# Optimization experiments

Hardware: AMD Instinct MI355X
Metric: run time of the kernel (lower is better)

Reference implementation:

```python
import jax, jax.numpy as jnp
import numpy as np

B, C, H, W = 4, 64, 64, 64
CI = C // 2  # inter_channels


def setup_inputs() -> dict:
    key = jax.random.key(0)
    k1, k2, k3, k4, k5 = jax.random.split(key, 5)
    x = jax.random.normal(k1, (B, C, H, W), dtype=jnp.float32)
    # 1x1 conv g: in C -> CI (weight [CI, C], bias [CI])
    Wg = jax.random.normal(k2, (CI, C), dtype=jnp.float32) * (1.0 / np.sqrt(C))
    bg = jax.random.normal(k3, (CI,), dtype=jnp.float32) * 0.01
    # 1x1 conv W_z: CI -> C
    Wz = jax.random.normal(k4, (C, CI), dtype=jnp.float32) * (1.0 / np.sqrt(CI))
    bz = jax.random.normal(k5, (C,), dtype=jnp.float32) * 0.01
    return {"x": x, "Wg": Wg, "bg": bg, "Wz": Wz, "bz": bz}


def reference(x, Wg, bg, Wz, bz):
    b, c, h, w = x.shape
    n = h * w
    xf = x.reshape(b, c, n)                       # [B,C,N]
    # g projection (1x1 conv) then flatten: [B,N,CI]
    g_x = jnp.einsum('bcn,oc->bno', xf, Wg) + bg  # [B,N,CI]
    # theta = phi = raw x flattened
    theta = xf.transpose(0, 2, 1)                 # [B,N,C]
    f = jnp.einsum('bnc,bcm->bnm', theta, xf)     # [B,N,N]
    f_div_C = jax.nn.softmax(f, axis=-1)
    y = jnp.einsum('bnm,bmo->bno', f_div_C, g_x)  # [B,N,CI]
    y = y.transpose(0, 2, 1).reshape(b, CI, h, w)  # [B,CI,H,W]
    # W_z projection (1x1 conv) + residual
    W_y = jnp.einsum('oi,bihw->bohw', Wz, y) + bz[None, :, None, None]
    return W_y + x
```

## Files before the change

kernel.cpp:

```cpp
#include <hip/hip_runtime.h>
#include <hip/hip_bf16.h>
#include <math.h>

#define B_  4
#define C_  64
#define N_  4096
#define CI_ 32

typedef __attribute__((ext_vector_type(8))) unsigned short u16x8;
typedef __attribute__((ext_vector_type(8))) __bf16        bf16x8;
typedef __attribute__((ext_vector_type(4))) __bf16        bf16x4;
typedef __attribute__((ext_vector_type(4))) float         f32x4;

__device__ __forceinline__ unsigned short f2bf(float f) {
    union { float f; unsigned int i; } v; v.f = f;
    unsigned int r = v.i + 0x7FFFu + ((v.i >> 16) & 1u);
    return (unsigned short)(r >> 16);
}

__global__ __launch_bounds__(256) void k_prep(
    const float* __restrict__ x, const float* __restrict__ Wg,
    const float* __restrict__ bg, unsigned short* __restrict__ xT,
    unsigned short* __restrict__ gx, float* __restrict__ diag)
{
    __shared__ __align__(16) float tile[64][68];
    __shared__ float part[4][64][33];
    const int t  = threadIdx.x;
    const int b  = blockIdx.x >> 6;
    const int n0 = (blockIdx.x & 63) * 64;

    #pragma unroll
    for (int pass = 0; pass < 4; ++pass) {
        int c   = (t >> 4) + pass * 16;
        int nl4 = (t & 15) * 4;
        float4 v = *(const float4*)(x + (size_t)(b * C_ + c) * N_ + n0 + nl4);
        *(float4*)&tile[c][nl4] = v;
    }
    __syncthreads();

    {
        const int n  = t >> 2;
        const int cc = (t & 3) * 16;
        u16x8 a, b2;
        #pragma unroll
        for (int j = 0; j < 8; ++j) a[j]  = f2bf(tile[cc + j][n]);
        #pragma unroll
        for (int j = 0; j < 8; ++j) b2[j] = f2bf(tile[cc + 8 + j][n]);
        unsigned short* dst = xT + (size_t)(b * N_ + n0 + n) * C_ + cc;
        *(u16x8*)dst       = a;
        *(u16x8*)(dst + 8) = b2;
    }
    {
        const int nl = t & 63, cq = t >> 6;
        float acc[CI_];
        #pragma unroll
        for (int o = 0; o < CI_; ++o) acc[o] = 0.f;
        float dd = 0.f;
        #pragma unroll 4
        for (int cl = 0; cl < 16; ++cl) {
            int c = cq * 16 + cl;
            float xv = tile[c][nl];
            dd += xv * xv;
            #pragma unroll
            for (int o = 0; o < CI_; ++o) acc[o] += Wg[o * C_ + c] * xv;
        }
        #pragma unroll
        for (int o = 0; o < CI_; ++o) part[cq][nl][o] = acc[o];
        part[cq][nl][32] = dd;
    }
    __syncthreads();
    {
        const int o = t >> 3, nr = (t & 7) * 8;
        u16x8 w;
        #pragma unroll
        for (int j = 0; j < 8; ++j) {
            int n = nr + j;
            float s = part[0][n][o] + part[1][n][o] + part[2][n][o] + part[3][n][o]
                    + bg[o];
            w[j] = f2bf(s);
        }
        *(u16x8*)(gx + (size_t)(b * CI_ + o) * N_ + n0 + nr) = w;
    }
    if (t < 64)
        diag[(size_t)b * N_ + n0 + t] =
            part[0][t][32] + part[1][t][32] + part[2][t][32] + part[3][t][32];
}

__device__ __forceinline__ f32x4 mfma16(bf16x8 a, bf16x8 b, f32x4 c) {
    return __builtin_amdgcn_mfma_f32_16x16x32_bf16(a, b, c, 0, 0, 0);
}

#define LOADA(Adst, koff)                                                      \
    _Pragma("unroll")                                                          \
    for (int kt = 0; kt < 2; ++kt) {                                           \
        _Pragma("unroll")                                                      \
        for (int kc = 0; kc < 2; ++kc)                                         \
            Adst[kt][kc] = *(const bf16x8*)(aBase                              \
                + (size_t)((koff) + kt * 16) * C_ + kc * 32);                  \
    }

#define LOADB(Bdst, koff)                                                      \
    Bdst[0] = *(const bf16x8*)(bBase0 + (koff));                               \
    Bdst[1] = *(const bf16x8*)(bBase1 + (koff));

#define TILE(Ar, Br, POFF)                                                     \
    {                                                                          \
        f32x4 S[2][2];                                                         \
        _Pragma("unroll")                                                      \
        for (int kt = 0; kt < 2; ++kt) {                                       \
            _Pragma("unroll")                                                  \
            for (int qt = 0; qt < 2; ++qt) {                                   \
                f32x4 z = (f32x4){nKq[qt], nKq[qt], nKq[qt], nKq[qt]};         \
                z = mfma16(Ar[kt][0], Qf[qt][0], z);                           \
                S[kt][qt] = mfma16(Ar[kt][1], Qf[qt][1], z);                   \
            }                                                                  \
        }                                                                      \
        _Pragma("unroll")                                                      \
        for (int qt = 0; qt < 2; ++qt) {                                       \
            _Pragma("unroll")                                                  \
            for (int kt = 0; kt < 2; ++kt) {                                   \
                bf16x4 pb;                                                     \
                _Pragma("unroll")                                              \
                for (int r = 0; r < 4; ++r) {                                  \
                    float p = __expf(S[kt][qt][r]);                            \
                    lacc[qt] += p;                                             \
                    pb[r] = (__bf16)p;                                         \
                }                                                              \
                *(bf16x4*)(pW + (POFF) + qt * 640 + kt * 16) = pb;             \
            }                                                                  \
        }                                                                      \
        bf16x8 Ap[2];                                                          \
        _Pragma("unroll")                                                      \
        for (int qt = 0; qt < 2; ++qt)                                         \
            Ap[qt] = *(const bf16x8*)(pR + (POFF) + qt * 640);                 \
        _Pragma("unroll")                                                      \
        for (int qt = 0; qt < 2; ++qt) {                                       \
            _Pragma("unroll")                                                  \
            for (int ot = 0; ot < 2; ++ot)                                     \
                Yf[qt][ot] = mfma16(Ap[qt], Br[ot], Yf[qt][ot]);               \
        }                                                                      \
    }

__global__ __launch_bounds__(256, 4) void k_flash(
    const unsigned short* __restrict__ xT, const unsigned short* __restrict__ gx,
    const float* __restrict__ diag,
    float* __restrict__ ypart, float* __restrict__ lpart)
{
    __shared__ __align__(16) char smem[20480];
    unsigned short* Pl = (unsigned short*)smem;

    const int tid  = threadIdx.x;
    const int wave = tid >> 6, lane = tid & 63;
    const int quad = lane >> 4, li = lane & 15;
    const int g = wave >> 1, qh = wave & 1;
    const int bi  = blockIdx.x;
    const int kq  = bi & 3;
    const int qtb = (bi >> 2) & 63;
    const int b   = bi >> 8;
    const int qw  = qtb * 64 + qh * 32;

    const unsigned short* xb = xT + (size_t)b * N_ * C_;
    const unsigned short* gb = gx + (size_t)b * CI_ * N_;

    float nKq[2];
    #pragma unroll
    for (int qt = 0; qt < 2; ++qt)
        nKq[qt] = -diag[(size_t)b * N_ + qw + qt * 16 + li];

    bf16x8 Qf[2][2];
    #pragma unroll
    for (int qt = 0; qt < 2; ++qt)
        #pragma unroll
        for (int kc = 0; kc < 2; ++kc)
            Qf[qt][kc] = *(const bf16x8*)(xb + (size_t)(qw + qt * 16 + li) * C_
                                          + kc * 32 + quad * 8);

    f32x4 Yf[2][2];
    #pragma unroll
    for (int qt = 0; qt < 2; ++qt)
        #pragma unroll
        for (int ot = 0; ot < 2; ++ot)
            Yf[qt][ot] = (f32x4){0.f, 0.f, 0.f, 0.f};
    float lacc[2] = {0.f, 0.f};

    const int keybase = kq * 1024 + g * 512;

    const unsigned short* aBase  = xb + (size_t)(keybase + li) * C_ + quad * 8;
    const unsigned short* bBase0 = gb + (size_t)(li) * N_      + keybase + quad * 8;
    const unsigned short* bBase1 = gb + (size_t)(16 + li) * N_ + keybase + quad * 8;
    unsigned short*       pW = Pl + (wave * 32 + li) * 40 + quad * 4;
    const unsigned short* pR = Pl + (wave * 32 + li) * 40 + quad * 8;

    bf16x8 A0[2][2], A1[2][2], B0v[2], B1v[2];
    LOADA(A0, 0)
    LOADB(B0v, 0)

    #pragma unroll 1
    for (int t2 = 0; t2 < 8; ++t2) {
        const int kodd = t2 * 64 + 32;
        LOADA(A1, kodd)
        LOADB(B1v, kodd)
        TILE(A0, B0v, 0)
        if (t2 < 7) {
            const int kev = t2 * 64 + 64;
            LOADA(A0, kev)
            LOADB(B0v, kev)
        }
        TILE(A1, B1v, 5120)
    }

    #pragma unroll
    for (int qt = 0; qt < 2; ++qt) {
        lacc[qt] += __shfl_xor(lacc[qt], 16, 64);
        lacc[qt] += __shfl_xor(lacc[qt], 32, 64);
    }

    __syncthreads();
    float* ym = (float*)smem;

    #pragma unroll
    for (int qt = 0; qt < 2; ++qt) {
        #pragma unroll
        for (int ot = 0; ot < 2; ++ot)
            #pragma unroll
            for (int r = 0; r < 4; ++r)
                ym[(wave * 32 + qt * 16 + quad * 4 + r) * 34 + ot * 16 + li] = Yf[qt][ot][r];
        if (quad == 0)
            ym[(wave * 32 + qt * 16 + li) * 34 + 32] = lacc[qt];
    }
    __syncthreads();
    {
        const int q = tid >> 2, og = tid & 3;
        const int qh2 = q >> 5, ql = q & 31;
        const int w0 = qh2, w1 = 2 + qh2;
        const size_t pbase = (size_t)(b * 64 + qtb) * 4 + kq;
        float* yp = ypart + pbase * 2048 + q * 32;
        #pragma unroll
        for (int j = 0; j < 8; ++j) {
            int o = og * 8 + j;
            yp[o] = ym[(w0 * 32 + ql) * 34 + o] + ym[(w1 * 32 + ql) * 34 + o];
        }
        if (og == 0)
            lpart[pbase * 64 + q] = ym[(w0 * 32 + ql) * 34 + 32]
                                  + ym[(w1 * 32 + ql) * 34 + 32];
    }
}

__global__ __launch_bounds__(256) void k_merge(
    const float* __restrict__ ypart, const float* __restrict__ lpart,
    const float* __restrict__ x, const float* __restrict__ Wz,
    const float* __restrict__ bz, float* __restrict__ out)
{
    __shared__ float yfin[64][33];
    const int t   = threadIdx.x;
    const int b   = blockIdx.x >> 6;
    const int qtb = blockIdx.x & 63;
    const int q0  = qtb * 64;

    {
        const int q = t >> 2, og = t & 3;
        const size_t pb = (size_t)(b * 64 + qtb) * 4;
        float l = lpart[(pb + 0) * 64 + q] + lpart[(pb + 1) * 64 + q]
                + lpart[(pb + 2) * 64 + q] + lpart[(pb + 3) * 64 + q];
        float inv = 1.f / l;
        #pragma unroll
        for (int j = 0; j < 8; ++j) {
            int o = og * 8 + j;
            float acc = 0.f;
            #pragma unroll
            for (int kq = 0; kq < 4; ++kq)
                acc += ypart[(pb + kq) * 2048 + q * 32 + o];
            yfin[q][o] = acc * inv;
        }
    }
    __syncthreads();
    {
        const int q = t & 63, c0 = t >> 6;
        #pragma unroll
        for (int i = 0; i < 16; ++i) {
            int cout = c0 + i * 4;
            float acc = bz[cout];
            #pragma unroll
            for (int o = 0; o < CI_; ++o)
                acc += Wz[cout * CI_ + o] * yfin[q][o];
            size_t oidx = (size_t)(b * C_ + cout) * N_ + q0 + q;
            out[oidx] = acc + x[oidx];
        }
    }
}

extern "C" void kernel_launch(void* const* d_in, const int* in_sizes, int n_in,
                              void* d_out, int out_size, void* d_ws, size_t ws_size,
                              hipStream_t stream) {
    (void)in_sizes; (void)n_in; (void)out_size; (void)ws_size;
    const float* x  = (const float*)d_in[0];
    const float* Wg = (const float*)d_in[1];
    const float* bg = (const float*)d_in[2];
    const float* Wz = (const float*)d_in[3];
    const float* bz = (const float*)d_in[4];
    float* out = (float*)d_out;

    unsigned short* xT = (unsigned short*)d_ws;
    unsigned short* gx = (unsigned short*)((char*)d_ws + 2097152);
    float* diag  = (float*)((char*)d_ws + 3145728);
    float* ypart = (float*)((char*)d_ws + 3211264);
    float* lpart = (float*)((char*)d_ws + 11599872);

    hipLaunchKernelGGL(k_prep,  dim3(B_ * (N_ / 64)),    dim3(256), 0, stream, x, Wg, bg, xT, gx, diag);
    hipLaunchKernelGGL(k_flash, dim3(B_ * 64 * 4),       dim3(256), 0, stream, xT, gx, diag, ypart, lpart);
    hipLaunchKernelGGL(k_merge, dim3(B_ * 64),           dim3(256), 0, stream, ypart, lpart, x, Wz, bz, out);
}
```

Measured before the change: 134.9 us.

## Stage key tiles through double-buffered LDS shared by wave pairs

Key tiles of x are now loaded cooperatively into padded, double-buffered shared memory, and both waves in a group read from that copy. Before, each wave loaded its own key fragments directly from global memory, so the same key data was fetched twice. The change halves global key traffic per block. In exchange it adds LDS traffic, two block-wide barriers per iteration and more shared memory, which may lower occupancy. The P buffer is no longer double-buffered.

```diff
diff --git a/kernel.cpp b/kernel.cpp
--- a/kernel.cpp
+++ b/kernel.cpp
@@ -90,29 +90,36 @@
     return __builtin_amdgcn_mfma_f32_16x16x32_bf16(a, b, c, 0, 0, 0);
 }
 
-#define LOADA(Adst, koff)                                                      \
-    _Pragma("unroll")                                                          \
-    for (int kt = 0; kt < 2; ++kt) {                                           \
-        _Pragma("unroll")                                                      \
-        for (int kc = 0; kc < 2; ++kc)                                         \
-            Adst[kt][kc] = *(const bf16x8*)(aBase                              \
-                + (size_t)((koff) + kt * 16) * C_ + kc * 32);                  \
-    }
-
-#define LOADB(Bdst, koff)                                                      \
-    Bdst[0] = *(const bf16x8*)(bBase0 + (koff));                               \
-    Bdst[1] = *(const bf16x8*)(bBase1 + (koff));
-
-#define TILE(Ar, Br, POFF)                                                     \
+#define KLOAD(kr, tT)                                                          \
+    kr[0] = *(const u16x8*)(kSrc0 + (size_t)(tT) * (32 * C_));                 \
+    kr[1] = *(const u16x8*)(kSrc1 + (size_t)(tT) * (32 * C_));
+
+#define KSTORE(bufS, kr)                                                       \
+    *(u16x8*)((bufS) + kDst0) = kr[0];                                         \
+    *(u16x8*)((bufS) + kDst1) = kr[1];
+
+#define VLOAD(vr, tT)                                                          \
+    vr[0] = *(const bf16x8*)(bBase0 + (tT) * 32);                              \
+    vr[1] = *(const bf16x8*)(bBase1 + (tT) * 32);
+
+#define COMPUTE(ABUF, Vr)                                                      \
     {                                                                          \
+        bf16x8 Af[2][2];                                                       \
+        _Pragma("unroll")                                                      \
+        for (int kt = 0; kt < 2; ++kt) {                                       \
+            _Pragma("unroll")                                                  \
+            for (int kc = 0; kc < 2; ++kc)                                     \
+                Af[kt][kc] = *(const bf16x8*)((ABUF)                           \
+                    + (g * 32 + kt * 16 + li) * 72 + kc * 32 + quad * 8);      \
+        }                                                                      \
         f32x4 S[2][2];                                                         \
         _Pragma("unroll")                                                      \
         for (int kt = 0; kt < 2; ++kt) {                                       \
             _Pragma("unroll")                                                  \
             for (int qt = 0; qt < 2; ++qt) {                                   \
                 f32x4 z = (f32x4){nKq[qt], nKq[qt], nKq[qt], nKq[qt]};         \
-                z = mfma16(Ar[kt][0], Qf[qt][0], z);                           \
-                S[kt][qt] = mfma16(Ar[kt][1], Qf[qt][1], z);                   \
+                z = mfma16(Af[kt][0], Qf[qt][0], z);                           \
+                S[kt][qt] = mfma16(Af[kt][1], Qf[qt][1], z);                   \
             }                                                                  \
         }                                                                      \
         _Pragma("unroll")                                                      \
@@ -126,18 +133,18 @@
                     lacc[qt] += p;                                             \
                     pb[r] = (__bf16)p;                                         \
                 }                                                              \
-                *(bf16x4*)(pW + (POFF) + qt * 640 + kt * 16) = pb;             \
+                *(bf16x4*)(pW + qt * 640 + kt * 16) = pb;                      \
             }                                                                  \
         }                                                                      \
         bf16x8 Ap[2];                                                          \
         _Pragma("unroll")                                                      \
         for (int qt = 0; qt < 2; ++qt)                                         \
-            Ap[qt] = *(const bf16x8*)(pR + (POFF) + qt * 640);                 \
+            Ap[qt] = *(const bf16x8*)(pR + qt * 640);                          \
         _Pragma("unroll")                                                      \
         for (int qt = 0; qt < 2; ++qt) {                                       \
             _Pragma("unroll")                                                  \
             for (int ot = 0; ot < 2; ++ot)                                     \
-                Yf[qt][ot] = mfma16(Ap[qt], Br[ot], Yf[qt][ot]);               \
+                Yf[qt][ot] = mfma16(Ap[qt], Vr[ot], Yf[qt][ot]);               \
         }                                                                      \
     }
 
@@ -146,8 +153,10 @@
     const float* __restrict__ diag,
     float* __restrict__ ypart, float* __restrict__ lpart)
 {
-    __shared__ __align__(16) char smem[20480];
-    unsigned short* Pl = (unsigned short*)smem;
+    __shared__ __align__(16) char smem[28672];
+    unsigned short* xk0 = (unsigned short*)smem;
+    unsigned short* xk1 = (unsigned short*)(smem + 9216);
+    unsigned short* Pl  = (unsigned short*)(smem + 18432);
 
     const int tid  = threadIdx.x;
     const int wave = tid >> 6, lane = tid & 63;
@@ -158,6 +167,7 @@
     const int qtb = (bi >> 2) & 63;
     const int b   = bi >> 8;
     const int qw  = qtb * 64 + qh * 32;
+    const int u   = tid & 127;
 
     const unsigned short* xb = xT + (size_t)b * N_ * C_;
     const unsigned short* gb = gx + (size_t)b * CI_ * N_;
@@ -184,29 +194,43 @@
     float lacc[2] = {0.f, 0.f};
 
     const int keybase = kq * 1024 + g * 512;
-
-    const unsigned short* aBase  = xb + (size_t)(keybase + li) * C_ + quad * 8;
+    const int gg = tid >> 7;
+    const int sbase = kq * 1024 + gg * 512;
+
+    const int cc0 = u * 2,      key0 = cc0 >> 3, cof0 = (cc0 & 7) * 8;
+    const int cc1 = u * 2 + 1,  key1 = cc1 >> 3, cof1 = (cc1 & 7) * 8;
+    const unsigned short* kSrc0 = xb + (size_t)(sbase + key0) * C_ + cof0;
+    const unsigned short* kSrc1 = xb + (size_t)(sbase + key1) * C_ + cof1;
+    const int kDst0 = (gg * 32 + key0) * 72 + cof0;
+    const int kDst1 = (gg * 32 + key1) * 72 + cof1;
+
     const unsigned short* bBase0 = gb + (size_t)(li) * N_      + keybase + quad * 8;
     const unsigned short* bBase1 = gb + (size_t)(16 + li) * N_ + keybase + quad * 8;
+
     unsigned short*       pW = Pl + (wave * 32 + li) * 40 + quad * 4;
     const unsigned short* pR = Pl + (wave * 32 + li) * 40 + quad * 8;
 
-    bf16x8 A0[2][2], A1[2][2], B0v[2], B1v[2];
-    LOADA(A0, 0)
-    LOADB(B0v, 0)
+    u16x8  kA[2], kB[2];
+    bf16x8 vA[2], vB[2];
+    KLOAD(kA, 0) VLOAD(vA, 0)
+    KLOAD(kB, 1) VLOAD(vB, 1)
+    KSTORE(xk0, kA)
+    KLOAD(kA, 2)
+    __syncthreads();
 
     #pragma unroll 1
     for (int t2 = 0; t2 < 8; ++t2) {
-        const int kodd = t2 * 64 + 32;
-        LOADA(A1, kodd)
-        LOADB(B1v, kodd)
-        TILE(A0, B0v, 0)
-        if (t2 < 7) {
-            const int kev = t2 * 64 + 64;
-            LOADA(A0, kev)
-            LOADB(B0v, kev)
-        }
-        TILE(A1, B1v, 5120)
+        const int te = 2 * t2;
+        KSTORE(xk1, kB)
+        COMPUTE(xk0, vA)
+        { const int nk = (te + 3 < 16) ? te + 3 : 15; KLOAD(kB, nk) }
+        { const int nv = (te + 2 < 16) ? te + 2 : 15; VLOAD(vA, nv) }
+        __syncthreads();
+        if (t2 < 7) { KSTORE(xk0, kA) }
+        COMPUTE(xk1, vB)
+        { const int nk = (te + 4 < 16) ? te + 4 : 15; KLOAD(kA, nk) }
+        { const int nv = (te + 3 < 16) ? te + 3 : 15; VLOAD(vB, nv) }
+        __syncthreads();
     }
 
     #pragma unroll
@@ -215,7 +239,6 @@
         lacc[qt] += __shfl_xor(lacc[qt], 32, 64);
     }
 
-    __syncthreads();
     float* ym = (float*)smem;
 
     #pragma unroll
```

After: 114.0 us. -15.5%, faster.

## Prefetch next key/value tiles inside tile compute with wave priority hints

Applied to the files above, without the earlier changes.

Restructures the flash loop so each tile body issues the loads for the tile two steps ahead right after its last use of the registers: key loads follow the QK MFMAs and value loads follow the PV MFMAs. It also drops the double-buffered P scratch in LDS (shared memory shrinks) and wraps the MFMA sections in s_setprio raises. The aim is to hide global load latency behind exp/convert work and to favour waves issuing matrix ops. The last iteration reloads redundant addresses instead of skipping them, adding some wasted load traffic. Reusing a single P buffer depends on per-wave ordering of LDS accesses.

```diff
diff --git a/kernel.cpp b/kernel.cpp
--- a/kernel.cpp
+++ b/kernel.cpp
@@ -90,22 +90,23 @@
     return __builtin_amdgcn_mfma_f32_16x16x32_bf16(a, b, c, 0, 0, 0);
 }
 
-#define LOADA(Adst, koff)                                                      \
+#define LOADA(Ad, koff)                                                        \
     _Pragma("unroll")                                                          \
     for (int kt = 0; kt < 2; ++kt) {                                           \
         _Pragma("unroll")                                                      \
         for (int kc = 0; kc < 2; ++kc)                                         \
-            Adst[kt][kc] = *(const bf16x8*)(aBase                              \
+            Ad[kt][kc] = *(const bf16x8*)(aBase                                \
                 + (size_t)((koff) + kt * 16) * C_ + kc * 32);                  \
     }
 
-#define LOADB(Bdst, koff)                                                      \
-    Bdst[0] = *(const bf16x8*)(bBase0 + (koff));                               \
-    Bdst[1] = *(const bf16x8*)(bBase1 + (koff));
-
-#define TILE(Ar, Br, POFF)                                                     \
+#define LOADV(Vd, koff)                                                        \
+    Vd[0] = *(const bf16x8*)(bBase0 + (koff));                                 \
+    Vd[1] = *(const bf16x8*)(bBase1 + (koff));
+
+#define TILEC(Ar, Vr, kpre)                                                    \
     {                                                                          \
         f32x4 S[2][2];                                                         \
+        __builtin_amdgcn_s_setprio(1);                                         \
         _Pragma("unroll")                                                      \
         for (int kt = 0; kt < 2; ++kt) {                                       \
             _Pragma("unroll")                                                  \
@@ -115,6 +116,8 @@
                 S[kt][qt] = mfma16(Ar[kt][1], Qf[qt][1], z);                   \
             }                                                                  \
         }                                                                      \
+        __builtin_amdgcn_s_setprio(0);                                         \
+        LOADA(Ar, kpre)                   \
         _Pragma("unroll")                                                      \
         for (int qt = 0; qt < 2; ++qt) {                                       \
             _Pragma("unroll")                                                  \
@@ -126,19 +129,22 @@
                     lacc[qt] += p;                                             \
                     pb[r] = (__bf16)p;                                         \
                 }                                                              \
-                *(bf16x4*)(pW + (POFF) + qt * 640 + kt * 16) = pb;             \
+                *(bf16x4*)(pW + qt * 640 + kt * 16) = pb;                      \
             }                                                                  \
         }                                                                      \
         bf16x8 Ap[2];                                                          \
         _Pragma("unroll")                                                      \
         for (int qt = 0; qt < 2; ++qt)                                         \
-            Ap[qt] = *(const bf16x8*)(pR + (POFF) + qt * 640);                 \
+            Ap[qt] = *(const bf16x8*)(pR + qt * 640);                          \
+        __builtin_amdgcn_s_setprio(1);                                         \
         _Pragma("unroll")                                                      \
         for (int qt = 0; qt < 2; ++qt) {                                       \
             _Pragma("unroll")                                                  \
             for (int ot = 0; ot < 2; ++ot)                                     \
-                Yf[qt][ot] = mfma16(Ap[qt], Br[ot], Yf[qt][ot]);               \
+                Yf[qt][ot] = mfma16(Ap[qt], Vr[ot], Yf[qt][ot]);               \
         }                                                                      \
+        __builtin_amdgcn_s_setprio(0);                                         \
+        LOADV(Vr, kpre)                   \
     }
 
 __global__ __launch_bounds__(256, 4) void k_flash(
@@ -146,7 +152,7 @@
     const float* __restrict__ diag,
     float* __restrict__ ypart, float* __restrict__ lpart)
 {
-    __shared__ __align__(16) char smem[20480];
+    __shared__ __align__(16) char smem[17408];
     unsigned short* Pl = (unsigned short*)smem;
 
     const int tid  = threadIdx.x;
@@ -191,22 +197,20 @@
     unsigned short*       pW = Pl + (wave * 32 + li) * 40 + quad * 4;
     const unsigned short* pR = Pl + (wave * 32 + li) * 40 + quad * 8;
 
-    bf16x8 A0[2][2], A1[2][2], B0v[2], B1v[2];
-    LOADA(A0, 0)
-    LOADB(B0v, 0)
+    bf16x8 A0[2][2], A1[2][2], V0[2], V1[2];
+    LOADA(A0, 0)  LOADV(V0, 0)
+    LOADA(A1, 32) LOADV(V1, 32)
+    asm volatile("" ::: "memory");
 
     #pragma unroll 1
     for (int t2 = 0; t2 < 8; ++t2) {
-        const int kodd = t2 * 64 + 32;
-        LOADA(A1, kodd)
-        LOADB(B1v, kodd)
-        TILE(A0, B0v, 0)
-        if (t2 < 7) {
-            const int kev = t2 * 64 + 64;
-            LOADA(A0, kev)
-            LOADB(B0v, kev)
-        }
-        TILE(A1, B1v, 5120)
+        const int ke  = t2 * 64;
+        const int kp0 = (t2 < 7) ? ke + 64 : ke;
+        const int kp1 = (t2 < 7) ? ke + 96 : ke + 32;
+        TILEC(A0, V0, kp0)
+        asm volatile("" ::: "memory");
+        TILEC(A1, V1, kp1)
+        asm volatile("" ::: "memory");
     }
 
     #pragma unroll
@@ -216,6 +220,7 @@
     }
 
     __syncthreads();
+
     float* ym = (float*)smem;
 
     #pragma unroll
```

After: 156.5 us. 1.16x slower.
